# Performance work log

Measured on AMD Instinct MI355X. Metric: run time of the kernel, lower is better.

## Reference

```python
import jax, jax.numpy as jnp
import numpy as np


def setup_inputs() -> dict:
    key = jax.random.key(0)
    k1, k2 = jax.random.split(key)
    x = jax.random.normal(k1, (8, 128, 128, 128), dtype=jnp.float32)        # [N, C, H, W]
    codebook = jax.random.normal(k2, (256, 128), dtype=jnp.float32)         # [K, C] class_emb_vecs
    return {"x": x, "codebook": codebook}


def reference(x, codebook):
    # Brute-force 1-NN with p=2 (Euclidean), matching sklearn NearestNeighbors(brute, p=2).
    # argmin ||q - c||_2 == argmin (||q||^2 - 2 q.c + ||c||^2), so use the GEMM form.
    N, C, H, W = x.shape
    q = jnp.transpose(x, (0, 2, 3, 1)).reshape(-1, C)       # [N*H*W, C], matches x.reshape(-1, C) channel-last? 
    # NOTE: torch x.reshape(-1, C) on [N,C,H,W] flattens with C as the fastest-varying of the
    # leading dims only when memory layout is NCHW -> rows are (n, c_blocks)... Torch's
    # reshape(-1, C) actually slices contiguous groups of C elements along W. To be faithful
    # to x.reshape(-1, C) on a contiguous NCHW tensor:
    q = x.reshape(-1, C)                                     # [N*C*H*W/C, C] — same elements, same order as torch
    q_sq = jnp.sum(q * q, axis=1, keepdims=True)             # [M, 1]
    c_sq = jnp.sum(codebook * codebook, axis=1)              # [K]
    # squared distances: [M, K]
    d2 = q_sq - 2.0 * (q @ codebook.T) + c_sq[None, :]
    idx = jnp.argmin(d2, axis=1).astype(jnp.int32)           # [M]
    return idx.reshape(N, H, W)
```

## Files before the change

kernel.cpp:

```cpp
#include <hip/hip_runtime.h>
#include <hip/hip_bf16.h>


typedef __bf16 bf16x8 __attribute__((ext_vector_type(8)));
typedef float  floatx4 __attribute__((ext_vector_type(4)));

#define MFMA16 __builtin_amdgcn_mfma_f32_16x16x32_bf16

#define CNT_OFF 0
#define CSQ_OFF 1024
#define CBB_OFF 4096
#define WL_OFF  (4096 + 131072)
#define WL_CAP  32768
#define T_FLAG  0.004f

__device__ __forceinline__ unsigned fmap(float f) {
    unsigned u = __float_as_uint(f);
    return (u & 0x80000000u) ? ~u : (u | 0x80000000u);
}
__device__ __forceinline__ float unfmap(unsigned u) {
    unsigned b = (u & 0x80000000u) ? (u ^ 0x80000000u) : ~u;
    return __uint_as_float(b);
}

__global__ void knn_prep(const float* __restrict__ cb, __bf16* __restrict__ cbB,
                         float* __restrict__ csq, int* __restrict__ cnt) {
    const int tid = threadIdx.x;
    const int id = blockIdx.x * 256 + tid;
    if (id == 0) *cnt = 0;
    const int part = id >> 12;
    const int rem = id & 4095;
    const int t4 = rem >> 8;
    const int kb = (rem >> 6) & 3;
    const int ln = id & 63;
    const int n = t4 * 16 + (ln & 15);
    const int k0 = kb * 32 + (ln >> 4) * 8;
    const float* src = cb + (size_t)n * 128 + k0;
    union { __bf16 h[8]; uint4 u; } p;
#pragma unroll
    for (int j = 0; j < 8; ++j) {
        float f = src[j];
        __bf16 hh = (__bf16)f;
        p.h[j] = (part == 0) ? hh : (__bf16)(f - (float)hh);
    }
    *(uint4*)(cbB + (size_t)id * 8) = p.u;

    if (blockIdx.x == 0) {
        const float4* row = (const float4*)(cb + (size_t)tid * 128);
        float a0 = 0.f, a1 = 0.f, a2 = 0.f, a3 = 0.f;
#pragma unroll 8
        for (int j = 0; j < 32; ++j) {
            float4 v = row[j];
            a0 = fmaf(v.x, v.x, a0);
            a1 = fmaf(v.y, v.y, a1);
            a2 = fmaf(v.z, v.z, a2);
            a3 = fmaf(v.w, v.w, a3);
        }
        csq[tid] = (a0 + a1) + (a2 + a3);
    }
}

__global__ __launch_bounds__(256, 2) void knn_mfma(const float* __restrict__ x,
                                                   const __bf16* __restrict__ cbB,
                                                   const float* __restrict__ csq_g,
                                                   int* __restrict__ out,
                                                   int* __restrict__ cnt,
                                                   int* __restrict__ wl) {
    __shared__ __bf16 sB[32768];
    __shared__ float s_csq[256];
    __shared__ unsigned long long sWb[128];
    __shared__ unsigned long long sWs[128];

    const int tid = threadIdx.x;
    const int wave = tid >> 6;
    const int lane = tid & 63;
    const int mg = wave >> 1;
    const int ng = wave & 1;
    const int rl = lane & 15;
    const int kg = lane >> 4;

    s_csq[tid] = csq_g[tid];

    const float* xq = x + ((size_t)blockIdx.x * 64 + mg * 32) * 128;
    bf16x8 ah[2][4], al[2][4];
#pragma unroll
    for (int m = 0; m < 2; ++m) {
#pragma unroll
        for (int kb = 0; kb < 4; ++kb) {
            const float* s = xq + (size_t)(m * 16 + rl) * 128 + kb * 32 + kg * 8;
            float4 f0 = *(const float4*)(s);
            float4 f1 = *(const float4*)(s + 4);
            float f[8] = {f0.x, f0.y, f0.z, f0.w, f1.x, f1.y, f1.z, f1.w};
            union { __bf16 h[8]; bf16x8 v; } ph, pl;
#pragma unroll
            for (int j = 0; j < 8; ++j) {
                __bf16 hh = (__bf16)f[j];
                ph.h[j] = hh;
                pl.h[j] = (__bf16)(f[j] - (float)hh);
            }
            ah[m][kb] = ph.v;
            al[m][kb] = pl.v;
        }
    }

    {
        const uint4* src = (const uint4*)cbB;
        uint4* dst = (uint4*)sB;
#pragma unroll 4
        for (int i = 0; i < 16; ++i) dst[i * 256 + tid] = src[i * 256 + tid];
    }
    __syncthreads();

    floatx4 acc[2][8];
#pragma unroll
    for (int m = 0; m < 2; ++m)
#pragma unroll
        for (int t = 0; t < 8; ++t) acc[m][t] = (floatx4){0.f, 0.f, 0.f, 0.f};

#pragma unroll
    for (int kb = 0; kb < 4; ++kb) {
#pragma unroll
        for (int t = 0; t < 8; ++t) {
            const int t4 = ng * 8 + t;
            bf16x8 b = *(const bf16x8*)(sB + (((t4 * 4 + kb) * 64 + lane) * 8));
            acc[0][t] = MFMA16(ah[0][kb], b, acc[0][t], 0, 0, 0);
            acc[1][t] = MFMA16(ah[1][kb], b, acc[1][t], 0, 0, 0);
            acc[0][t] = MFMA16(al[0][kb], b, acc[0][t], 0, 0, 0);
            acc[1][t] = MFMA16(al[1][kb], b, acc[1][t], 0, 0, 0);
        }
    }
    __syncthreads();

    {
        const uint4* src = (const uint4*)(cbB + 32768);
        uint4* dst = (uint4*)sB;
#pragma unroll 4
        for (int i = 0; i < 16; ++i) dst[i * 256 + tid] = src[i * 256 + tid];
    }
    __syncthreads();

#pragma unroll
    for (int kb = 0; kb < 4; ++kb) {
#pragma unroll
        for (int t = 0; t < 8; ++t) {
            const int t4 = ng * 8 + t;
            bf16x8 b = *(const bf16x8*)(sB + (((t4 * 4 + kb) * 64 + lane) * 8));
            acc[0][t] = MFMA16(ah[0][kb], b, acc[0][t], 0, 0, 0);
            acc[1][t] = MFMA16(ah[1][kb], b, acc[1][t], 0, 0, 0);
        }
    }

    float cs[8];
#pragma unroll
    for (int t = 0; t < 8; ++t) cs[t] = s_csq[(ng * 8 + t) * 16 + rl];

#pragma unroll
    for (int m = 0; m < 2; ++m) {
#pragma unroll
        for (int r = 0; r < 4; ++r) {
            unsigned long long b = ~0ULL, s = ~0ULL;
#pragma unroll
            for (int t = 0; t < 8; ++t) {
                const int n = (ng * 8 + t) * 16 + rl;
                float score = fmaf(-2.0f, acc[m][t][r], cs[t]);
                unsigned long long key =
                    ((unsigned long long)fmap(score) << 32) | (unsigned)n;
                if (key < b) { s = b; b = key; }
                else if (key < s) { s = key; }
            }
#pragma unroll
            for (int d = 1; d < 16; d <<= 1) {
                unsigned long long ob = __shfl_xor(b, d);
                unsigned long long os = __shfl_xor(s, d);
                unsigned long long nb = ob < b ? ob : b;
                unsigned long long mx = ob < b ? b : ob;
                unsigned long long mn = os < s ? os : s;
                b = nb;
                s = mx < mn ? mx : mn;
            }
            if (rl == 0) {
                const int ql = mg * 32 + m * 16 + kg * 4 + r;
                sWb[ql * 2 + ng] = b;
                sWs[ql * 2 + ng] = s;
            }
        }
    }
    __syncthreads();

    if (tid < 64) {
        unsigned long long b0 = sWb[tid * 2 + 0], b1 = sWb[tid * 2 + 1];
        unsigned long long s0 = sWs[tid * 2 + 0], s1 = sWs[tid * 2 + 1];
        unsigned long long best = b0 < b1 ? b0 : b1;
        unsigned long long mx = b0 < b1 ? b1 : b0;
        unsigned long long mn = s0 < s1 ? s0 : s1;
        unsigned long long sec = mx < mn ? mx : mn;
        const size_t qg = (size_t)blockIdx.x * 64 + tid;
        out[qg] = (int)(unsigned)(best & 0xFFFFFFFFull);
        float f1 = unfmap((unsigned)(best >> 32));
        float f2 = unfmap((unsigned)(sec >> 32));
        if (f2 - f1 < T_FLAG) {
            int idx = atomicAdd(cnt, 1);
            if (idx < WL_CAP) wl[idx] = (int)qg;
        }
    }
}

__global__ __launch_bounds__(256) void knn_refine(const float* __restrict__ x,
                                                  const float* __restrict__ cb,
                                                  const float* __restrict__ csq_g,
                                                  const int* __restrict__ wl,
                                                  const int* __restrict__ cnt,
                                                  int* __restrict__ out) {
    __shared__ unsigned long long sP[4];
    const int tid = threadIdx.x;
    const int lane = tid & 63;
    const int wave = tid >> 6;

    int n = *cnt;
    if (n > WL_CAP) n = WL_CAP;
    const float mycsq = csq_g[tid];
    const float4* cr = (const float4*)(cb + (size_t)tid * 128);

    for (int i = blockIdx.x; i < n; i += gridDim.x) {
        const int q = wl[i];
        const float4* qr = (const float4*)(x + (size_t)q * 128);
        float a0 = 0.f, a1 = 0.f, a2 = 0.f, a3 = 0.f;
#pragma unroll 8
        for (int c4 = 0; c4 < 32; ++c4) {
            float4 qv = qr[c4];
            float4 cv = cr[c4];
            a0 = fmaf(qv.x, cv.x, a0);
            a1 = fmaf(qv.y, cv.y, a1);
            a2 = fmaf(qv.z, cv.z, a2);
            a3 = fmaf(qv.w, cv.w, a3);
        }
        float dot = (a0 + a1) + (a2 + a3);
        float score = fmaf(-2.0f, dot, mycsq);
        unsigned long long key =
            ((unsigned long long)fmap(score) << 32) | (unsigned)tid;
#pragma unroll
        for (int d = 1; d < 64; d <<= 1) {
            unsigned long long o = __shfl_xor(key, d);
            key = o < key ? o : key;
        }
        if (lane == 0) sP[wave] = key;
        __syncthreads();
        if (tid == 0) {
            unsigned long long b = sP[0];
            unsigned long long o;
            o = sP[1]; b = o < b ? o : b;
            o = sP[2]; b = o < b ? o : b;
            o = sP[3]; b = o < b ? o : b;
            out[q] = (int)(unsigned)(b & 0xFFFFFFFFull);
        }
        __syncthreads();
    }
}

extern "C" void kernel_launch(void* const* d_in, const int* in_sizes, int n_in,
                              void* d_out, int out_size, void* d_ws, size_t ws_size,
                              hipStream_t stream) {
    const float* x = (const float*)d_in[0];
    const float* cb = (const float*)d_in[1];
    int* out = (int*)d_out;

    char* ws = (char*)d_ws;
    int* cnt = (int*)(ws + CNT_OFF);
    float* csq = (float*)(ws + CSQ_OFF);
    __bf16* cbB = (__bf16*)(ws + CBB_OFF);
    int* wl = (int*)(ws + WL_OFF);

    const int M = in_sizes[0] / 128;

    knn_prep<<<32, 256, 0, stream>>>(cb, cbB, csq, cnt);
    knn_mfma<<<M / 64, 256, 0, stream>>>(x, cbB, csq, out, cnt, wl);
    knn_refine<<<240, 256, 0, stream>>>(x, cb, csq, wl, cnt, out);
}
```

Baseline: 145.3 us.

## Fuse exact-refinement pass into MFMA kernel using per-block shared worklist

The separate refine kernel and global atomic worklist are removed. Each MFMA block now collects its ambiguous queries (top-2 gap below threshold) into a shared-memory list and recomputes their distances in fp32 right away. This saves one kernel launch, the global atomic counter and the worklist round trip, and it drops the worklist capacity cap. In exchange, blocks with many flagged queries run a serial loop with two block barriers per query, and that extra work sits on the MFMA kernel's critical path.

```diff
diff --git a/kernel.cpp b/kernel.cpp
--- a/kernel.cpp
+++ b/kernel.cpp
@@ -7,11 +7,8 @@
 
 #define MFMA16 __builtin_amdgcn_mfma_f32_16x16x32_bf16
 
-#define CNT_OFF 0
 #define CSQ_OFF 1024
 #define CBB_OFF 4096
-#define WL_OFF  (4096 + 131072)
-#define WL_CAP  32768
 #define T_FLAG  0.004f
 
 __device__ __forceinline__ unsigned fmap(float f) {
@@ -24,10 +21,9 @@
 }
 
 __global__ void knn_prep(const float* __restrict__ cb, __bf16* __restrict__ cbB,
-                         float* __restrict__ csq, int* __restrict__ cnt) {
+                         float* __restrict__ csq) {
     const int tid = threadIdx.x;
     const int id = blockIdx.x * 256 + tid;
-    if (id == 0) *cnt = 0;
     const int part = id >> 12;
     const int rem = id & 4095;
     const int t4 = rem >> 8;
@@ -61,15 +57,17 @@
 }
 
 __global__ __launch_bounds__(256, 2) void knn_mfma(const float* __restrict__ x,
+                                                   const float* __restrict__ cb,
                                                    const __bf16* __restrict__ cbB,
                                                    const float* __restrict__ csq_g,
-                                                   int* __restrict__ out,
-                                                   int* __restrict__ cnt,
-                                                   int* __restrict__ wl) {
+                                                   int* __restrict__ out) {
     __shared__ __bf16 sB[32768];
     __shared__ float s_csq[256];
     __shared__ unsigned long long sWb[128];
     __shared__ unsigned long long sWs[128];
+    __shared__ unsigned long long s_red[4];
+    __shared__ int s_nf;
+    __shared__ int s_flagq[64];
 
     const int tid = threadIdx.x;
     const int wave = tid >> 6;
@@ -80,6 +78,7 @@
     const int kg = lane >> 4;
 
     s_csq[tid] = csq_g[tid];
+    if (tid == 0) s_nf = 0;
 
     const float* xq = x + ((size_t)blockIdx.x * 64 + mg * 32) * 128;
     bf16x8 ah[2][4], al[2][4];
@@ -199,31 +198,18 @@
         float f1 = unfmap((unsigned)(best >> 32));
         float f2 = unfmap((unsigned)(sec >> 32));
         if (f2 - f1 < T_FLAG) {
-            int idx = atomicAdd(cnt, 1);
-            if (idx < WL_CAP) wl[idx] = (int)qg;
-        }
-    }
-}
-
-__global__ __launch_bounds__(256) void knn_refine(const float* __restrict__ x,
-                                                  const float* __restrict__ cb,
-                                                  const float* __restrict__ csq_g,
-                                                  const int* __restrict__ wl,
-                                                  const int* __restrict__ cnt,
-                                                  int* __restrict__ out) {
-    __shared__ unsigned long long sP[4];
-    const int tid = threadIdx.x;
-    const int lane = tid & 63;
-    const int wave = tid >> 6;
-
-    int n = *cnt;
-    if (n > WL_CAP) n = WL_CAP;
-    const float mycsq = csq_g[tid];
-    const float4* cr = (const float4*)(cb + (size_t)tid * 128);
-
-    for (int i = blockIdx.x; i < n; i += gridDim.x) {
-        const int q = wl[i];
-        const float4* qr = (const float4*)(x + (size_t)q * 128);
+            int i = atomicAdd(&s_nf, 1);
+            s_flagq[i] = tid;
+        }
+    }
+    __syncthreads();
+
+    const int nf = s_nf;
+    for (int i = 0; i < nf; ++i) {
+        const int lq = s_flagq[i];
+        const size_t q = (size_t)blockIdx.x * 64 + lq;
+        const float4* qr = (const float4*)(x + q * 128);
+        const float4* cr = (const float4*)(cb + (size_t)tid * 128);
         float a0 = 0.f, a1 = 0.f, a2 = 0.f, a3 = 0.f;
 #pragma unroll 8
         for (int c4 = 0; c4 < 32; ++c4) {
@@ -235,7 +221,7 @@
             a3 = fmaf(qv.w, cv.w, a3);
         }
         float dot = (a0 + a1) + (a2 + a3);
-        float score = fmaf(-2.0f, dot, mycsq);
+        float score = fmaf(-2.0f, dot, s_csq[tid]);
         unsigned long long key =
             ((unsigned long long)fmap(score) << 32) | (unsigned)tid;
 #pragma unroll
@@ -243,14 +229,14 @@
             unsigned long long o = __shfl_xor(key, d);
             key = o < key ? o : key;
         }
-        if (lane == 0) sP[wave] = key;
+        if (lane == 0) s_red[wave] = key;
         __syncthreads();
         if (tid == 0) {
-            unsigned long long b = sP[0];
+            unsigned long long b = s_red[0];
             unsigned long long o;
-            o = sP[1]; b = o < b ? o : b;
-            o = sP[2]; b = o < b ? o : b;
-            o = sP[3]; b = o < b ? o : b;
+            o = s_red[1]; b = o < b ? o : b;
+            o = s_red[2]; b = o < b ? o : b;
+            o = s_red[3]; b = o < b ? o : b;
             out[q] = (int)(unsigned)(b & 0xFFFFFFFFull);
         }
         __syncthreads();
@@ -265,14 +251,11 @@
     int* out = (int*)d_out;
 
     char* ws = (char*)d_ws;
-    int* cnt = (int*)(ws + CNT_OFF);
     float* csq = (float*)(ws + CSQ_OFF);
     __bf16* cbB = (__bf16*)(ws + CBB_OFF);
-    int* wl = (int*)(ws + WL_OFF);
 
     const int M = in_sizes[0] / 128;
 
-    knn_prep<<<32, 256, 0, stream>>>(cb, cbB, csq, cnt);
-    knn_mfma<<<M / 64, 256, 0, stream>>>(x, cbB, csq, out, cnt, wl);
-    knn_refine<<<240, 256, 0, stream>>>(x, cb, csq, wl, cnt, out);
-}
+    knn_prep<<<32, 256, 0, stream>>>(cb, cbB, csq);
+    knn_mfma<<<M / 64, 256, 0, stream>>>(x, cb, cbB, csq, out);
+}
```

Result: slower. 149.6 us (+2.9%).
